# Optimization experiments

Hardware: AMD Instinct MI355X
Metric: run time of the kernel (lower is better)

Reference implementation:

```python
import jax, jax.numpy as jnp
import numpy as np

N, E, B = 50000, 800000, 128
H, L, FIN, GF = 256, 4, 8, 85
LN_EPS = 1e-5


def _ln(x, g, b):
    m = jnp.mean(x, axis=-1, keepdims=True)
    v = jnp.var(x, axis=-1, keepdims=True)
    return g * (x - m) * jax.lax.rsqrt(v + LN_EPS) + b


def setup_inputs() -> dict:
    key = jax.random.key(0)
    ks = iter(jax.random.split(key, 40))

    def nrm(shape, scale):
        return jax.random.normal(next(ks), shape, jnp.float32) * scale

    inp = {}
    inp["x"] = nrm((N, FIN), 1.0)
    inp["edge_index"] = jax.random.randint(next(ks), (2, E), 0, N, dtype=jnp.int32)
    inp["edge_weight"] = jax.random.uniform(next(ks), (E,), jnp.float32)
    inp["batch"] = jnp.sort(jax.random.randint(next(ks), (N,), 0, B, dtype=jnp.int32))
    inp["gene_feat"] = nrm((B, GF), 1.0)
    # input projection
    inp["W_in"] = nrm((FIN, H), FIN ** -0.5); inp["b_in"] = jnp.zeros((H,), jnp.float32)
    inp["ln_in_g"] = jnp.ones((H,), jnp.float32); inp["ln_in_b"] = jnp.zeros((H,), jnp.float32)
    # GIN layers (stacked over L)
    inp["eps"] = jnp.zeros((L,), jnp.float32)
    inp["W1"] = nrm((L, H, 2 * H), H ** -0.5); inp["b1"] = jnp.zeros((L, 2 * H), jnp.float32)
    inp["W2"] = nrm((L, 2 * H, H), (2 * H) ** -0.5); inp["b2"] = jnp.zeros((L, H), jnp.float32)
    inp["ln_g"] = jnp.ones((L, H), jnp.float32); inp["ln_b"] = jnp.zeros((L, H), jnp.float32)
    # gene feature projection
    inp["Wg1"] = nrm((GF, H), GF ** -0.5); inp["bg1"] = jnp.zeros((H,), jnp.float32)
    inp["lng_g"] = jnp.ones((H,), jnp.float32); inp["lng_b"] = jnp.zeros((H,), jnp.float32)
    inp["Wg2"] = nrm((H, H // 2), H ** -0.5); inp["bg2"] = jnp.zeros((H // 2,), jnp.float32)
    # classifier (embed_dim = 2H + H//2 = 640)
    ED = 2 * H + H // 2
    inp["Wc1"] = nrm((ED, H), ED ** -0.5); inp["bc1"] = jnp.zeros((H,), jnp.float32)
    inp["Wc2"] = nrm((H, H // 2), H ** -0.5); inp["bc2"] = jnp.zeros((H // 2,), jnp.float32)
    inp["Wc3"] = nrm((H // 2, 2), (H // 2) ** -0.5); inp["bc3"] = jnp.zeros((2,), jnp.float32)
    return inp


def reference(x, edge_index, edge_weight, batch, gene_feat,
              W_in, b_in, ln_in_g, ln_in_b,
              eps, W1, b1, W2, b2, ln_g, ln_b,
              Wg1, bg1, lng_g, lng_b, Wg2, bg2,
              Wc1, bc1, Wc2, bc2, Wc3, bc3):
    n = x.shape[0]
    nb = gene_feat.shape[0]
    # input projection: Linear -> LayerNorm -> ReLU  (dropout = eval mode)
    h = jax.nn.relu(_ln(x @ W_in + b_in, ln_in_g, ln_in_b))
    src, dst = edge_index[0], edge_index[1]
    for i in range(W1.shape[0]):
        res = h
        # weighted GIN aggregation; self-loops with weight 1 fold into (2+eps)*h
        msg = h[src] * edge_weight[:, None]            # [E, H]
        agg = jax.ops.segment_sum(msg, dst, num_segments=n)
        out = (2.0 + eps[i]) * h + agg
        out = jax.nn.relu(out @ W1[i] + b1[i]) @ W2[i] + b2[i]
        h = jax.nn.relu(_ln(out, ln_g[i], ln_b[i])) + res
    # dual pooling (mean + max) per graph
    counts = jax.ops.segment_sum(jnp.ones((n,), h.dtype), batch, num_segments=nb)
    gmean = jax.ops.segment_sum(h, batch, num_segments=nb) / jnp.clip(counts, 1.0)[:, None]
    gmax = jax.ops.segment_max(h, batch, num_segments=nb)
    gmax = jnp.where(jnp.isfinite(gmax), gmax, 0.0)
    # gene feature projection
    gp = jax.nn.relu(_ln(gene_feat @ Wg1 + bg1, lng_g, lng_b))
    gp = jax.nn.relu(gp @ Wg2 + bg2)
    g = jnp.concatenate([gmean, gmax, gp], axis=-1)   # [B, 640]
    # classifier
    hc = jax.nn.relu(g @ Wc1 + bc1)
    hc = jax.nn.relu(hc @ Wc2 + bc2)
    return hc @ Wc3 + bc3
```

## Files before the change

### kernel.cpp

```cpp
#include <hip/hip_runtime.h>
#include <hip/hip_bf16.h>

#define N_NODES 50000
#define MP 50048
#define N_EDGES 800000
#define N_B 128
#define H_DIM 256
#define H2_DIM 512
#define FIN_DIM 8
#define GF_DIM 85
#define LN_EPS 1e-5f
#define SCAN_NBLK 196

typedef unsigned short u16;
typedef unsigned int u32;
typedef _Float16 f16;
typedef __attribute__((ext_vector_type(8))) _Float16 f16x8;
typedef __attribute__((ext_vector_type(8))) unsigned short u16x8;
typedef __attribute__((ext_vector_type(4))) float f32x4;

__device__ inline float relu_f(float x) { return x > 0.f ? x : 0.f; }

__device__ inline float h2f(u16 b) { f16 h; __builtin_memcpy(&h, &b, 2); return (float)h; }
__device__ inline u16 f2h(float x) { f16 h = (f16)x; u16 b; __builtin_memcpy(&b, &h, 2); return b; }

#define GLOAD16(gp, lp) __builtin_amdgcn_global_load_lds( \
    (const __attribute__((address_space(1))) void*)(gp),  \
    (__attribute__((address_space(3))) void*)(lp), 16, 0, 0)

__device__ inline void ln_stats_256(float v, float* sbuf, float& mean, float& rstd) {
    float s = v, s2 = v * v;
#pragma unroll
    for (int off = 32; off > 0; off >>= 1) {
        s += __shfl_down(s, off);
        s2 += __shfl_down(s2, off);
    }
    int t = threadIdx.x;
    if ((t & 63) == 0) { sbuf[t >> 6] = s; sbuf[4 + (t >> 6)] = s2; }
    __syncthreads();
    float ts = sbuf[0] + sbuf[1] + sbuf[2] + sbuf[3];
    float ts2 = sbuf[4] + sbuf[5] + sbuf[6] + sbuf[7];
    mean = ts * (1.f / H_DIM);
    float var = ts2 * (1.f / H_DIM) - mean * mean;
    rstd = rsqrtf(var + LN_EPS);
}

__global__ void k_input_proj(const float* __restrict__ x, const float* __restrict__ Wi,
                             const float* __restrict__ bi, const float* __restrict__ g,
                             const float* __restrict__ bb,
                             u16* __restrict__ Hh, u16* __restrict__ Hl) {
    int n = blockIdx.x, t = threadIdx.x;
    __shared__ float xs[FIN_DIM];
    __shared__ float sbuf[8];
    if (t < FIN_DIM) xs[t] = x[n * FIN_DIM + t];
    __syncthreads();
    float acc = bi[t];
#pragma unroll
    for (int k = 0; k < FIN_DIM; ++k) acc = fmaf(xs[k], Wi[k * H_DIM + t], acc);
    float mean, rstd;
    ln_stats_256(acc, sbuf, mean, rstd);
    float v = relu_f(g[t] * (acc - mean) * rstd + bb[t]);
    u16 hh = f2h(v);
    size_t o = (size_t)n * H_DIM + t;
    Hh[o] = hh;
    Hl[o] = f2h(v - h2f(hh));
}

__global__ void k_hist(const int* __restrict__ ei, int* __restrict__ deg) {
    int e = blockIdx.x * 256 + threadIdx.x;
    atomicAdd(&deg[ei[N_EDGES + e]], 1);
}

__global__ void k_scan1(const int* __restrict__ deg, int* __restrict__ row_start,
                        int* __restrict__ bsum) {
    __shared__ int s[256];
    int t = threadIdx.x, i = blockIdx.x * 256 + t;
    int v = (i < N_NODES) ? deg[i] : 0;
    s[t] = v;
    __syncthreads();
    for (int off = 1; off < 256; off <<= 1) {
        int x = (t >= off) ? s[t - off] : 0;
        __syncthreads();
        s[t] += x;
        __syncthreads();
    }
    if (i < N_NODES) row_start[i] = s[t] - v;
    if (t == 255) bsum[blockIdx.x] = s[255];
}

__global__ void k_scan2(int* __restrict__ bsum) {
    __shared__ int s[256];
    int t = threadIdx.x;
    int v = (t < SCAN_NBLK) ? bsum[t] : 0;
    s[t] = v;
    __syncthreads();
    for (int off = 1; off < 256; off <<= 1) {
        int x = (t >= off) ? s[t - off] : 0;
        __syncthreads();
        s[t] += x;
        __syncthreads();
    }
    if (t < SCAN_NBLK) bsum[t] = s[t] - v;
}

__global__ void k_scan3(int* __restrict__ row_start, const int* __restrict__ bsum) {
    int t = threadIdx.x, i = blockIdx.x * 256 + t;
    if (i < N_NODES) row_start[i] += bsum[blockIdx.x];
    if (i == 0) row_start[N_NODES] = N_EDGES;
}

__global__ void k_scatter(const int* __restrict__ ei, const float* __restrict__ ew,
                          const int* __restrict__ row_start, int* __restrict__ cursor,
                          int* __restrict__ csr_src, float* __restrict__ csr_w) {
    int e = blockIdx.x * 256 + threadIdx.x;
    int d = ei[N_EDGES + e];
    int p = atomicAdd(&cursor[d], 1);
    int i = row_start[d] + p;
    csr_src[i] = ei[e];
    csr_w[i] = ew[e];
}

__global__ void k_gbounds(const int* __restrict__ batch, int* __restrict__ gstart,
                          int* __restrict__ gcnt) {
    __shared__ int s[N_B + 1];
    int b = threadIdx.x;
    int lo = 0, hi = N_NODES;
    while (lo < hi) {
        int mid = (lo + hi) >> 1;
        if (batch[mid] < b) lo = mid + 1; else hi = mid;
    }
    s[b] = lo;
    if (b == 0) s[N_B] = N_NODES;
    __syncthreads();
    gstart[b] = s[b];
    gcnt[b] = s[b + 1] - s[b];
}

__global__ void k_agg(const u16* __restrict__ Hh, const u16* __restrict__ Hl,
                      const int* __restrict__ row_start,
                      const int* __restrict__ csr_src, const float* __restrict__ csr_w,
                      const float* __restrict__ eps, int layer,
                      u16* __restrict__ Ah) {
    const int n = blockIdx.x, t = threadIdx.x, wv = t >> 6, lane = t & 63;
    const int half = lane >> 5, sl = lane & 31;
    __shared__ int s_src[256];
    __shared__ float s_w[256];
    __shared__ float part[4][256];
    int start = row_start[n], end = row_start[n + 1];
    float a[8];
#pragma unroll
    for (int q = 0; q < 8; ++q) a[q] = 0.f;
    for (int e0 = start; e0 < end; e0 += 256) {
        int ne = end - e0; if (ne > 256) ne = 256;
        if (t < ne) { s_src[t] = csr_src[e0 + t]; s_w[t] = csr_w[e0 + t]; }
        __syncthreads();
        for (int j = wv * 2 + half; j < ne; j += 8) {
            int src = s_src[j];
            float w = s_w[j];
            u16x8 v = *reinterpret_cast<const u16x8*>(&Hh[(size_t)src * H_DIM + sl * 8]);
#pragma unroll
            for (int q = 0; q < 8; ++q) a[q] = fmaf(w, h2f(v[q]), a[q]);
        }
        __syncthreads();
    }
#pragma unroll
    for (int q = 0; q < 8; ++q) a[q] += __shfl_xor(a[q], 32);
    if (half == 0) {
        *reinterpret_cast<float4*>(&part[wv][sl * 8]) = (float4){a[0], a[1], a[2], a[3]};
        *reinterpret_cast<float4*>(&part[wv][sl * 8 + 4]) = (float4){a[4], a[5], a[6], a[7]};
    }
    __syncthreads();
    float sum = part[0][t] + part[1][t] + part[2][t] + part[3][t];
    size_t so = (size_t)n * H_DIM + t;
    float e2 = 2.0f + eps[layer];
    float hs = h2f(Hh[so]) + h2f(Hl[so]);
    Ah[so] = f2h(e2 * hs + sum);
}

__global__ void k_wprep(const float* __restrict__ W, u16* __restrict__ T, int R, int C) {
    __shared__ float tile[64][65];
    int c0 = blockIdx.x * 64, r0 = blockIdx.y * 64;
    const float* Wl = W + (size_t)blockIdx.z * R * C;
    u16* Tl_ = T + (size_t)blockIdx.z * R * C;
    int t = threadIdx.x;
    int col = t & 63, qr = t >> 6;
#pragma unroll
    for (int i = 0; i < 16; ++i) {
        int row = i * 4 + qr;
        tile[row][col] = Wl[(size_t)(r0 + row) * C + c0 + col];
    }
    __syncthreads();
#pragma unroll
    for (int i = 0; i < 16; ++i) {
        int crow = i * 4 + qr;
        Tl_[(size_t)(c0 + crow) * R + r0 + col] = f2h(tile[col][crow]);
    }
}

#define C1LD 520
__global__ __launch_bounds__(512, 2) void k_mlp(
    const u16* __restrict__ Ah, const u16* __restrict__ W1t, const u16* __restrict__ W2t,
    const float* __restrict__ b1v, const float* __restrict__ b2v,
    const float* __restrict__ lg, const float* __restrict__ lbv,
    const u16* __restrict__ Rh, const u16* __restrict__ Rl,
    u16* __restrict__ Oh, u16* __restrict__ Ol) {
    __shared__ __align__(16) u16 sA[64 * 32];
    __shared__ __align__(16) u16 sB[512 * 32];
    __shared__ __align__(16) u16 sC1[64 * C1LD];
    __shared__ float lnS[64][4], lnS2[64][4];
    __shared__ float lnm[64], lnr[64];
    const int t = threadIdx.x;
    const int wv = t >> 6, lane = t & 63;
    const int fr = lane & 15, kg = lane >> 4;
    const int cg = wv & 3, rg = wv >> 2;
    const int m0 = blockIdx.x * 64;

    f32x4 acc1[2][8];
#pragma unroll
    for (int i = 0; i < 2; ++i)
#pragma unroll
        for (int j = 0; j < 8; ++j) acc1[i][j] = (f32x4){0.f, 0.f, 0.f, 0.f};

    for (int k0 = 0; k0 < H_DIM; k0 += 32) {
        if (wv < 4) {
            int r = t >> 2, p = t & 3;
            GLOAD16(Ah + (size_t)(m0 + r) * H_DIM + k0 + p * 8, &sA[(wv * 64) * 8]);
        }
#pragma unroll
        for (int is = 0; is < 4; ++is) {
            int chunk = is * 512 + t;
            int r = chunk >> 2, p = chunk & 3;
            GLOAD16(W1t + (size_t)r * H_DIM + k0 + p * 8, &sB[(is * 512 + wv * 64) * 8]);
        }
        __syncthreads();
        f16x8 fa[2], fb[8];
#pragma unroll
        for (int mf = 0; mf < 2; ++mf)
            fa[mf] = *(const f16x8*)&sA[(rg * 32 + mf * 16 + fr) * 32 + kg * 8];
#pragma unroll
        for (int nf = 0; nf < 8; ++nf)
            fb[nf] = *(const f16x8*)&sB[(cg * 128 + nf * 16 + fr) * 32 + kg * 8];
#pragma unroll
        for (int mf = 0; mf < 2; ++mf)
#pragma unroll
            for (int nf = 0; nf < 8; ++nf)
                acc1[mf][nf] = __builtin_amdgcn_mfma_f32_16x16x32_f16(fa[mf], fb[nf], acc1[mf][nf], 0, 0, 0);
        __syncthreads();
    }
#pragma unroll
    for (int nf = 0; nf < 8; ++nf) {
        int col = cg * 128 + nf * 16 + fr;
        float bi = b1v[col];
#pragma unroll
        for (int mf = 0; mf < 2; ++mf)
#pragma unroll
            for (int j = 0; j < 4; ++j) {
                int row = rg * 32 + mf * 16 + kg * 4 + j;
                sC1[row * C1LD + col] = f2h(relu_f(acc1[mf][nf][j] + bi));
            }
    }
    __syncthreads();

    f32x4 acc2[2][4];
#pragma unroll
    for (int i = 0; i < 2; ++i)
#pragma unroll
        for (int j = 0; j < 4; ++j) acc2[i][j] = (f32x4){0.f, 0.f, 0.f, 0.f};

    for (int k0 = 0; k0 < H2_DIM; k0 += 32) {
#pragma unroll
        for (int is = 0; is < 2; ++is) {
            int chunk = is * 512 + t;
            int r = chunk >> 2, p = chunk & 3;
            GLOAD16(W2t + (size_t)r * H2_DIM + k0 + p * 8, &sB[(is * 512 + wv * 64) * 8]);
        }
        __syncthreads();
        f16x8 fa[2], fb[4];
#pragma unroll
        for (int mf = 0; mf < 2; ++mf)
            fa[mf] = *(const f16x8*)&sC1[(rg * 32 + mf * 16 + fr) * C1LD + k0 + kg * 8];
#pragma unroll
        for (int nf = 0; nf < 4; ++nf)
            fb[nf] = *(const f16x8*)&sB[(cg * 64 + nf * 16 + fr) * 32 + kg * 8];
#pragma unroll
        for (int mf = 0; mf < 2; ++mf)
#pragma unroll
            for (int nf = 0; nf < 4; ++nf)
                acc2[mf][nf] = __builtin_amdgcn_mfma_f32_16x16x32_f16(fa[mf], fb[nf], acc2[mf][nf], 0, 0, 0);
        __syncthreads();
    }
    float bcol[4];
#pragma unroll
    for (int nf = 0; nf < 4; ++nf) bcol[nf] = b2v[cg * 64 + nf * 16 + fr];
#pragma unroll
    for (int mf = 0; mf < 2; ++mf)
#pragma unroll
        for (int nf = 0; nf < 4; ++nf)
#pragma unroll
            for (int j = 0; j < 4; ++j) acc2[mf][nf][j] += bcol[nf];
#pragma unroll
    for (int mf = 0; mf < 2; ++mf)
#pragma unroll
        for (int j = 0; j < 4; ++j) {
            float s = acc2[mf][0][j] + acc2[mf][1][j] + acc2[mf][2][j] + acc2[mf][3][j];
            float s2 = acc2[mf][0][j] * acc2[mf][0][j] + acc2[mf][1][j] * acc2[mf][1][j] +
                       acc2[mf][2][j] * acc2[mf][2][j] + acc2[mf][3][j] * acc2[mf][3][j];
#pragma unroll
            for (int off = 1; off < 16; off <<= 1) {
                s += __shfl_xor(s, off);
                s2 += __shfl_xor(s2, off);
            }
            if (fr == 0) {
                int row = rg * 32 + mf * 16 + kg * 4 + j;
                lnS[row][cg] = s;
                lnS2[row][cg] = s2;
            }
        }
    __syncthreads();
    if (t < 64) {
        float s = lnS[t][0] + lnS[t][1] + lnS[t][2] + lnS[t][3];
        float s2 = lnS2[t][0] + lnS2[t][1] + lnS2[t][2] + lnS2[t][3];
        float m = s * (1.f / 256.f);
        float var = s2 * (1.f / 256.f) - m * m;
        lnm[t] = m;
        lnr[t] = rsqrtf(var + LN_EPS);
    }
    __syncthreads();
    float gg[4], bb[4];
#pragma unroll
    for (int nf = 0; nf < 4; ++nf) {
        int col = cg * 64 + nf * 16 + fr;
        gg[nf] = lg[col];
        bb[nf] = lbv[col];
    }
#pragma unroll
    for (int mf = 0; mf < 2; ++mf)
#pragma unroll
        for (int j = 0; j < 4; ++j) {
            int row = rg * 32 + mf * 16 + kg * 4 + j;
            int grow = m0 + row;
            float m = lnm[row], rs = lnr[row];
#pragma unroll
            for (int nf = 0; nf < 4; ++nf) {
                int col = cg * 64 + nf * 16 + fr;
                size_t o = (size_t)grow * H_DIM + col;
                float res = h2f(Rh[o]) + h2f(Rl[o]);
                float v = relu_f(gg[nf] * (acc2[mf][nf][j] - m) * rs + bb[nf]) + res;
                u16 hh = f2h(v);
                Oh[o] = hh;
                Ol[o] = f2h(v - h2f(hh));
            }
        }
}

__global__ void k_pool(const u16* __restrict__ Hh, const u16* __restrict__ Hl,
                       const int* __restrict__ gstart,
                       const int* __restrict__ gcnt, float* __restrict__ g) {
    int b = blockIdx.x;
    int col = blockIdx.y * 64 + (threadIdx.x & 63);
    int r = threadIdx.x >> 6;
    int st = gstart[b], cnt = gcnt[b];
    float s = 0.f, mx = -3.4e38f;
    for (int i = r; i < cnt; i += 4) {
        size_t o = (size_t)(st + i) * H_DIM + col;
        float v = h2f(Hh[o]) + h2f(Hl[o]);
        s += v;
        mx = fmaxf(mx, v);
    }
    __shared__ float ss[256], sm[256];
    ss[threadIdx.x] = s;
    sm[threadIdx.x] = mx;
    __syncthreads();
    if (r == 0) {
#pragma unroll
        for (int k = 1; k < 4; ++k) {
            s += ss[threadIdx.x + 64 * k];
            mx = fmaxf(mx, sm[threadIdx.x + 64 * k]);
        }
        float mean = cnt > 0 ? s / (float)cnt : 0.f;
        if (cnt == 0) mx = 0.f;
        g[b * 640 + col] = mean;
        g[b * 640 + 256 + col] = mx;
    }
}

__global__ void k_gene(const float* __restrict__ gf, const float* __restrict__ Wg1,
                       const float* __restrict__ bg1, const float* __restrict__ lg,
                       const float* __restrict__ lb, const float* __restrict__ Wg2,
                       const float* __restrict__ bg2, float* __restrict__ g) {
    int b = blockIdx.x, t = threadIdx.x;
    __shared__ float xs[GF_DIM];
    __shared__ float sbuf[8];
    __shared__ float s1[H_DIM];
    if (t < GF_DIM) xs[t] = gf[b * GF_DIM + t];
    __syncthreads();
    float acc = bg1[t];
    for (int k = 0; k < GF_DIM; ++k) acc = fmaf(xs[k], Wg1[k * H_DIM + t], acc);
    float mean, rstd;
    ln_stats_256(acc, sbuf, mean, rstd);
    s1[t] = relu_f(lg[t] * (acc - mean) * rstd + lb[t]);
    __syncthreads();
    if (t < 128) {
        float a2 = bg2[t];
        for (int k = 0; k < H_DIM; ++k) a2 = fmaf(s1[k], Wg2[k * 128 + t], a2);
        g[b * 640 + 512 + t] = relu_f(a2);
    }
}

__global__ void k_cls(const float* __restrict__ g, const float* __restrict__ Wc1,
                      const float* __restrict__ bc1, const float* __restrict__ Wc2,
                      const float* __restrict__ bc2, const float* __restrict__ Wc3,
                      const float* __restrict__ bc3, float* __restrict__ out) {
    int b = blockIdx.x, t = threadIdx.x;
    __shared__ float gg[640];
    __shared__ float s1[256];
    __shared__ float s2[128];
    gg[t] = g[b * 640 + t];
    gg[t + 256] = g[b * 640 + 256 + t];
    if (t < 128) gg[t + 512] = g[b * 640 + 512 + t];
    __syncthreads();
    float a = bc1[t];
    for (int k = 0; k < 640; ++k) a = fmaf(gg[k], Wc1[k * 256 + t], a);
    s1[t] = relu_f(a);
    __syncthreads();
    if (t < 128) {
        float a2 = bc2[t];
        for (int k = 0; k < 256; ++k) a2 = fmaf(s1[k], Wc2[k * 128 + t], a2);
        s2[t] = relu_f(a2);
    }
    __syncthreads();
    if (t < 2) {
        float a3 = bc3[t];
        for (int k = 0; k < 128; ++k) a3 = fmaf(s2[k], Wc3[k * 2 + t], a3);
        out[b * 2 + t] = a3;
    }
}

extern "C" void kernel_launch(void* const* d_in, const int* in_sizes, int n_in,
                              void* d_out, int out_size, void* d_ws, size_t ws_size,
                              hipStream_t stream) {
    const float* x = (const float*)d_in[0];
    const int* ei = (const int*)d_in[1];
    const float* ew = (const float*)d_in[2];
    const int* batch = (const int*)d_in[3];
    const float* gf = (const float*)d_in[4];
    const float* W_in = (const float*)d_in[5];
    const float* b_in = (const float*)d_in[6];
    const float* ln_in_g = (const float*)d_in[7];
    const float* ln_in_b = (const float*)d_in[8];
    const float* eps = (const float*)d_in[9];
    const float* W1 = (const float*)d_in[10];
    const float* b1 = (const float*)d_in[11];
    const float* W2 = (const float*)d_in[12];
    const float* b2 = (const float*)d_in[13];
    const float* ln_g = (const float*)d_in[14];
    const float* ln_b = (const float*)d_in[15];
    const float* Wg1 = (const float*)d_in[16];
    const float* bg1 = (const float*)d_in[17];
    const float* lng_g = (const float*)d_in[18];
    const float* lng_b = (const float*)d_in[19];
    const float* Wg2 = (const float*)d_in[20];
    const float* bg2 = (const float*)d_in[21];
    const float* Wc1 = (const float*)d_in[22];
    const float* bc1 = (const float*)d_in[23];
    const float* Wc2 = (const float*)d_in[24];
    const float* bc2 = (const float*)d_in[25];
    const float* Wc3 = (const float*)d_in[26];
    const float* bc3 = (const float*)d_in[27];
    float* out = (float*)d_out;

    char* ws = (char*)d_ws;
    size_t off = 0;
    auto alloc = [&](size_t bytes) -> char* {
        char* p = ws + off;
        off += (bytes + 255) & ~(size_t)255;
        return p;
    };
    u16* Hh0 = (u16*)alloc((size_t)MP * H_DIM * 2);
    u16* Hl0 = (u16*)alloc((size_t)MP * H_DIM * 2);
    u16* Hh1 = (u16*)alloc((size_t)MP * H_DIM * 2);
    u16* Hl1 = (u16*)alloc((size_t)MP * H_DIM * 2);
    u16* Ah = (u16*)alloc((size_t)MP * H_DIM * 2);
    u16* W1T = (u16*)alloc((size_t)4 * H2_DIM * H_DIM * 2);
    u16* W2T = (u16*)alloc((size_t)4 * H_DIM * H2_DIM * 2);
    int* deg = (int*)alloc(N_NODES * 4);
    int* cursor = (int*)alloc(N_NODES * 4);
    int* row_start = (int*)alloc((N_NODES + 1) * 4);
    int* bsum = (int*)alloc(256 * 4);
    int* gcnt = (int*)alloc(N_B * 4);
    int* gstart = (int*)alloc(N_B * 4);
    int* csr_src = (int*)alloc(N_EDGES * 4);
    float* csr_w = (float*)alloc(N_EDGES * 4);
    float* gbuf = (float*)alloc(N_B * 640 * 4);
    (void)ws_size; (void)in_sizes; (void)n_in; (void)out_size;

    hipMemsetAsync(deg, 0, (size_t)((char*)row_start - (char*)deg), stream);

    k_wprep<<<dim3(H2_DIM / 64, H_DIM / 64, 4), 256, 0, stream>>>(W1, W1T, H_DIM, H2_DIM);
    k_wprep<<<dim3(H_DIM / 64, H2_DIM / 64, 4), 256, 0, stream>>>(W2, W2T, H2_DIM, H_DIM);

    k_input_proj<<<N_NODES, 256, 0, stream>>>(x, W_in, b_in, ln_in_g, ln_in_b, Hh0, Hl0);
    k_hist<<<N_EDGES / 256, 256, 0, stream>>>(ei, deg);
    k_scan1<<<SCAN_NBLK, 256, 0, stream>>>(deg, row_start, bsum);
    k_scan2<<<1, 256, 0, stream>>>(bsum);
    k_scan3<<<SCAN_NBLK, 256, 0, stream>>>(row_start, bsum);
    k_scatter<<<N_EDGES / 256, 256, 0, stream>>>(ei, ew, row_start, cursor, csr_src, csr_w);
    k_gbounds<<<1, N_B, 0, stream>>>(batch, gstart, gcnt);

    u16* hch = Hh0; u16* hcl = Hl0;
    u16* hnh = Hh1; u16* hnl = Hl1;
    for (int l = 0; l < 4; ++l) {
        k_agg<<<N_NODES, 256, 0, stream>>>(hch, hcl, row_start, csr_src, csr_w, eps, l, Ah);
        k_mlp<<<MP / 64, 512, 0, stream>>>(
            Ah, W1T + (size_t)l * H2_DIM * H_DIM, W2T + (size_t)l * H_DIM * H2_DIM,
            b1 + (size_t)l * H2_DIM, b2 + (size_t)l * H_DIM,
            ln_g + (size_t)l * H_DIM, ln_b + (size_t)l * H_DIM,
            hch, hcl, hnh, hnl);
        u16* th = hch; hch = hnh; hnh = th;
        u16* tl = hcl; hcl = hnl; hnl = tl;
    }

    k_pool<<<dim3(N_B, 4), 256, 0, stream>>>(hch, hcl, gstart, gcnt, gbuf);
    k_gene<<<N_B, 256, 0, stream>>>(gf, Wg1, bg1, lng_g, lng_b, Wg2, bg2, gbuf);
    k_cls<<<N_B, 256, 0, stream>>>(gbuf, Wc1, bc1, Wc2, bc2, Wc3, bc3, out);
}
```

Measured before the change: 910.9 us.

## Halve MLP row tile to 32 and XOR-swizzle the intermediate LDS buffer

```diff
diff --git a/kernel.cpp b/kernel.cpp
--- a/kernel.cpp
+++ b/kernel.cpp
@@ -197,34 +197,32 @@
     }
 }
 
-#define C1LD 520
+#define C1IDX(row, k) (((row) * 512 + (k)) ^ (((row) & 7) << 3))
 __global__ __launch_bounds__(512, 2) void k_mlp(
     const u16* __restrict__ Ah, const u16* __restrict__ W1t, const u16* __restrict__ W2t,
     const float* __restrict__ b1v, const float* __restrict__ b2v,
     const float* __restrict__ lg, const float* __restrict__ lbv,
     const u16* __restrict__ Rh, const u16* __restrict__ Rl,
     u16* __restrict__ Oh, u16* __restrict__ Ol) {
-    __shared__ __align__(16) u16 sA[64 * 32];
+    __shared__ __align__(16) u16 sA[32 * 32];
     __shared__ __align__(16) u16 sB[512 * 32];
-    __shared__ __align__(16) u16 sC1[64 * C1LD];
-    __shared__ float lnS[64][4], lnS2[64][4];
-    __shared__ float lnm[64], lnr[64];
+    __shared__ __align__(16) u16 sC1[32 * 512];
+    __shared__ float lnS[32][4], lnS2[32][4];
+    __shared__ float lnm[32], lnr[32];
     const int t = threadIdx.x;
     const int wv = t >> 6, lane = t & 63;
     const int fr = lane & 15, kg = lane >> 4;
     const int cg = wv & 3, rg = wv >> 2;
-    const int m0 = blockIdx.x * 64;
-
-    f32x4 acc1[2][8];
-#pragma unroll
-    for (int i = 0; i < 2; ++i)
-#pragma unroll
-        for (int j = 0; j < 8; ++j) acc1[i][j] = (f32x4){0.f, 0.f, 0.f, 0.f};
+    const int m0 = blockIdx.x * 32;
+
+    f32x4 acc1[8];
+#pragma unroll
+    for (int j = 0; j < 8; ++j) acc1[j] = (f32x4){0.f, 0.f, 0.f, 0.f};
 
     for (int k0 = 0; k0 < H_DIM; k0 += 32) {
-        if (wv < 4) {
+        if (t < 128) {
             int r = t >> 2, p = t & 3;
-            GLOAD16(Ah + (size_t)(m0 + r) * H_DIM + k0 + p * 8, &sA[(wv * 64) * 8]);
+            GLOAD16(Ah + (size_t)(m0 + r) * H_DIM + k0 + p * 8, &sA[wv * 512]);
         }
 #pragma unroll
         for (int is = 0; is < 4; ++is) {
@@ -233,18 +231,14 @@
             GLOAD16(W1t + (size_t)r * H_DIM + k0 + p * 8, &sB[(is * 512 + wv * 64) * 8]);
         }
         __syncthreads();
-        f16x8 fa[2], fb[8];
-#pragma unroll
-        for (int mf = 0; mf < 2; ++mf)
-            fa[mf] = *(const f16x8*)&sA[(rg * 32 + mf * 16 + fr) * 32 + kg * 8];
+        f16x8 fa, fb[8];
+        fa = *(const f16x8*)&sA[(rg * 16 + fr) * 32 + kg * 8];
 #pragma unroll
         for (int nf = 0; nf < 8; ++nf)
             fb[nf] = *(const f16x8*)&sB[(cg * 128 + nf * 16 + fr) * 32 + kg * 8];
 #pragma unroll
-        for (int mf = 0; mf < 2; ++mf)
-#pragma unroll
-            for (int nf = 0; nf < 8; ++nf)
-                acc1[mf][nf] = __builtin_amdgcn_mfma_f32_16x16x32_f16(fa[mf], fb[nf], acc1[mf][nf], 0, 0, 0);
+        for (int nf = 0; nf < 8; ++nf)
+            acc1[nf] = __builtin_amdgcn_mfma_f32_16x16x32_f16(fa, fb[nf], acc1[nf], 0, 0, 0);
         __syncthreads();
     }
 #pragma unroll
@@ -252,20 +246,16 @@
         int col = cg * 128 + nf * 16 + fr;
         float bi = b1v[col];
 #pragma unroll
-        for (int mf = 0; mf < 2; ++mf)
-#pragma unroll
-            for (int j = 0; j < 4; ++j) {
-                int row = rg * 32 + mf * 16 + kg * 4 + j;
-                sC1[row * C1LD + col] = f2h(relu_f(acc1[mf][nf][j] + bi));
-            }
-    }
-    __syncthreads();
-
-    f32x4 acc2[2][4];
-#pragma unroll
-    for (int i = 0; i < 2; ++i)
-#pragma unroll
-        for (int j = 0; j < 4; ++j) acc2[i][j] = (f32x4){0.f, 0.f, 0.f, 0.f};
+        for (int j = 0; j < 4; ++j) {
+            int row = rg * 16 + kg * 4 + j;
+            sC1[C1IDX(row, col)] = f2h(relu_f(acc1[nf][j] + bi));
+        }
+    }
+    __syncthreads();
+
+    f32x4 acc2[4];
+#pragma unroll
+    for (int j = 0; j < 4; ++j) acc2[j] = (f32x4){0.f, 0.f, 0.f, 0.f};
 
     for (int k0 = 0; k0 < H2_DIM; k0 += 32) {
 #pragma unroll
@@ -275,49 +265,44 @@
             GLOAD16(W2t + (size_t)r * H2_DIM + k0 + p * 8, &sB[(is * 512 + wv * 64) * 8]);
         }
         __syncthreads();
-        f16x8 fa[2], fb[4];
-#pragma unroll
-        for (int mf = 0; mf < 2; ++mf)
-            fa[mf] = *(const f16x8*)&sC1[(rg * 32 + mf * 16 + fr) * C1LD + k0 + kg * 8];
+        f16x8 fa, fb[4];
+        {
+            int row = rg * 16 + fr;
+            fa = *(const f16x8*)&sC1[C1IDX(row, k0 + kg * 8)];
+        }
 #pragma unroll
         for (int nf = 0; nf < 4; ++nf)
             fb[nf] = *(const f16x8*)&sB[(cg * 64 + nf * 16 + fr) * 32 + kg * 8];
 #pragma unroll
-        for (int mf = 0; mf < 2; ++mf)
-#pragma unroll
-            for (int nf = 0; nf < 4; ++nf)
-                acc2[mf][nf] = __builtin_amdgcn_mfma_f32_16x16x32_f16(fa[mf], fb[nf], acc2[mf][nf], 0, 0, 0);
+        for (int nf = 0; nf < 4; ++nf)
+            acc2[nf] = __builtin_amdgcn_mfma_f32_16x16x32_f16(fa, fb[nf], acc2[nf], 0, 0, 0);
         __syncthreads();
     }
     float bcol[4];
 #pragma unroll
     for (int nf = 0; nf < 4; ++nf) bcol[nf] = b2v[cg * 64 + nf * 16 + fr];
 #pragma unroll
-    for (int mf = 0; mf < 2; ++mf)
-#pragma unroll
-        for (int nf = 0; nf < 4; ++nf)
-#pragma unroll
-            for (int j = 0; j < 4; ++j) acc2[mf][nf][j] += bcol[nf];
-#pragma unroll
-    for (int mf = 0; mf < 2; ++mf)
-#pragma unroll
-        for (int j = 0; j < 4; ++j) {
-            float s = acc2[mf][0][j] + acc2[mf][1][j] + acc2[mf][2][j] + acc2[mf][3][j];
-            float s2 = acc2[mf][0][j] * acc2[mf][0][j] + acc2[mf][1][j] * acc2[mf][1][j] +
-                       acc2[mf][2][j] * acc2[mf][2][j] + acc2[mf][3][j] * acc2[mf][3][j];
-#pragma unroll
-            for (int off = 1; off < 16; off <<= 1) {
-                s += __shfl_xor(s, off);
-                s2 += __shfl_xor(s2, off);
-            }
-            if (fr == 0) {
-                int row = rg * 32 + mf * 16 + kg * 4 + j;
-                lnS[row][cg] = s;
-                lnS2[row][cg] = s2;
-            }
-        }
-    __syncthreads();
-    if (t < 64) {
+    for (int nf = 0; nf < 4; ++nf)
+#pragma unroll
+        for (int j = 0; j < 4; ++j) acc2[nf][j] += bcol[nf];
+#pragma unroll
+    for (int j = 0; j < 4; ++j) {
+        float s = acc2[0][j] + acc2[1][j] + acc2[2][j] + acc2[3][j];
+        float s2 = acc2[0][j] * acc2[0][j] + acc2[1][j] * acc2[1][j] +
+                   acc2[2][j] * acc2[2][j] + acc2[3][j] * acc2[3][j];
+#pragma unroll
+        for (int off = 1; off < 16; off <<= 1) {
+            s += __shfl_xor(s, off);
+            s2 += __shfl_xor(s2, off);
+        }
+        if (fr == 0) {
+            int row = rg * 16 + kg * 4 + j;
+            lnS[row][cg] = s;
+            lnS2[row][cg] = s2;
+        }
+    }
+    __syncthreads();
+    if (t < 32) {
         float s = lnS[t][0] + lnS[t][1] + lnS[t][2] + lnS[t][3];
         float s2 = lnS2[t][0] + lnS2[t][1] + lnS2[t][2] + lnS2[t][3];
         float m = s * (1.f / 256.f);
@@ -334,23 +319,21 @@
         bb[nf] = lbv[col];
     }
 #pragma unroll
-    for (int mf = 0; mf < 2; ++mf)
-#pragma unroll
-        for (int j = 0; j < 4; ++j) {
-            int row = rg * 32 + mf * 16 + kg * 4 + j;
-            int grow = m0 + row;
-            float m = lnm[row], rs = lnr[row];
-#pragma unroll
-            for (int nf = 0; nf < 4; ++nf) {
-                int col = cg * 64 + nf * 16 + fr;
-                size_t o = (size_t)grow * H_DIM + col;
-                float res = h2f(Rh[o]) + h2f(Rl[o]);
-                float v = relu_f(gg[nf] * (acc2[mf][nf][j] - m) * rs + bb[nf]) + res;
-                u16 hh = f2h(v);
-                Oh[o] = hh;
-                Ol[o] = f2h(v - h2f(hh));
-            }
-        }
+    for (int j = 0; j < 4; ++j) {
+        int row = rg * 16 + kg * 4 + j;
+        int grow = m0 + row;
+        float m = lnm[row], rs = lnr[row];
+#pragma unroll
+        for (int nf = 0; nf < 4; ++nf) {
+            int col = cg * 64 + nf * 16 + fr;
+            size_t o = (size_t)grow * H_DIM + col;
+            float res = h2f(Rh[o]) + h2f(Rl[o]);
+            float v = relu_f(gg[nf] * (acc2[nf][j] - m) * rs + bb[nf]) + res;
+            u16 hh = f2h(v);
+            Oh[o] = hh;
+            Ol[o] = f2h(v - h2f(hh));
+        }
+    }
 }
 
 __global__ void k_pool(const u16* __restrict__ Hh, const u16* __restrict__ Hl,
@@ -511,7 +494,7 @@
     u16* hnh = Hh1; u16* hnl = Hl1;
     for (int l = 0; l < 4; ++l) {
         k_agg<<<N_NODES, 256, 0, stream>>>(hch, hcl, row_start, csr_src, csr_w, eps, l, Ah);
-        k_mlp<<<MP / 64, 512, 0, stream>>>(
+        k_mlp<<<MP / 32, 512, 0, stream>>>(
             Ah, W1T + (size_t)l * H2_DIM * H_DIM, W2T + (size_t)l * H_DIM * H2_DIM,
             b1 + (size_t)l * H2_DIM, b2 + (size_t)l * H_DIM,
             ln_g + (size_t)l * H_DIM, ln_b + (size_t)l * H_DIM,
```

Result: faster. 872.7 us (-4.2%).

## Restructure fused MLP: 32-row tiles, weights straight from global, swizzled LDS

Applied to the files above, without the earlier changes.

```diff
diff --git a/kernel.cpp b/kernel.cpp
--- a/kernel.cpp
+++ b/kernel.cpp
@@ -197,139 +197,139 @@
     }
 }
 
-#define C1LD 520
+#define C1IDX(row, k) (((row) * 512 + (k)) ^ (((row) & 7) << 3))
 __global__ __launch_bounds__(512, 2) void k_mlp(
     const u16* __restrict__ Ah, const u16* __restrict__ W1t, const u16* __restrict__ W2t,
     const float* __restrict__ b1v, const float* __restrict__ b2v,
     const float* __restrict__ lg, const float* __restrict__ lbv,
     const u16* __restrict__ Rh, const u16* __restrict__ Rl,
     u16* __restrict__ Oh, u16* __restrict__ Ol) {
-    __shared__ __align__(16) u16 sA[64 * 32];
-    __shared__ __align__(16) u16 sB[512 * 32];
-    __shared__ __align__(16) u16 sC1[64 * C1LD];
-    __shared__ float lnS[64][4], lnS2[64][4];
-    __shared__ float lnm[64], lnr[64];
+    __shared__ __align__(16) u16 sA[32 * 256];
+    __shared__ __align__(16) u16 sC1[32 * 512];
+    __shared__ float lnS[32][8], lnS2[32][8];
+    __shared__ float lnm[32], lnr[32];
     const int t = threadIdx.x;
     const int wv = t >> 6, lane = t & 63;
     const int fr = lane & 15, kg = lane >> 4;
-    const int cg = wv & 3, rg = wv >> 2;
-    const int m0 = blockIdx.x * 64;
-
-    f32x4 acc1[2][8];
+    const int m0 = blockIdx.x * 32;
+
+#pragma unroll
+    for (int i = 0; i < 2; ++i) {
+        int chunk = i * 512 + t;
+        int r = chunk >> 5, c = chunk & 31;
+        GLOAD16(Ah + (size_t)(m0 + r) * H_DIM + ((c ^ (r & 7)) << 3),
+                &sA[(i * 512 + wv * 64) * 8]);
+    }
+    __syncthreads();
+
+    f32x4 acc1[2][4];
 #pragma unroll
     for (int i = 0; i < 2; ++i)
 #pragma unroll
-        for (int j = 0; j < 8; ++j) acc1[i][j] = (f32x4){0.f, 0.f, 0.f, 0.f};
-
-    for (int k0 = 0; k0 < H_DIM; k0 += 32) {
-        if (wv < 4) {
-            int r = t >> 2, p = t & 3;
-            GLOAD16(Ah + (size_t)(m0 + r) * H_DIM + k0 + p * 8, &sA[(wv * 64) * 8]);
-        }
-#pragma unroll
-        for (int is = 0; is < 4; ++is) {
-            int chunk = is * 512 + t;
-            int r = chunk >> 2, p = chunk & 3;
-            GLOAD16(W1t + (size_t)r * H_DIM + k0 + p * 8, &sB[(is * 512 + wv * 64) * 8]);
-        }
-        __syncthreads();
-        f16x8 fa[2], fb[8];
+        for (int j = 0; j < 4; ++j) acc1[i][j] = (f32x4){0.f, 0.f, 0.f, 0.f};
+
+#pragma unroll 2
+    for (int step = 0; step < 8; ++step) {
+        int k0 = step * 32;
+        f16x8 fa[2], fb[4];
+#pragma unroll
+        for (int mf = 0; mf < 2; ++mf) {
+            int row = mf * 16 + fr;
+            int cc = (step * 4 + kg) ^ (row & 7);
+            fa[mf] = *(const f16x8*)&sA[row * 256 + cc * 8];
+        }
+#pragma unroll
+        for (int nf = 0; nf < 4; ++nf) {
+            int col = wv * 64 + nf * 16 + fr;
+            fb[nf] = *(const f16x8*)&W1t[(size_t)col * H_DIM + k0 + kg * 8];
+        }
 #pragma unroll
         for (int mf = 0; mf < 2; ++mf)
-            fa[mf] = *(const f16x8*)&sA[(rg * 32 + mf * 16 + fr) * 32 + kg * 8];
-#pragma unroll
-        for (int nf = 0; nf < 8; ++nf)
-            fb[nf] = *(const f16x8*)&sB[(cg * 128 + nf * 16 + fr) * 32 + kg * 8];
+#pragma unroll
+            for (int nf = 0; nf < 4; ++nf)
+                acc1[mf][nf] = __builtin_amdgcn_mfma_f32_16x16x32_f16(fa[mf], fb[nf], acc1[mf][nf], 0, 0, 0);
+    }
+#pragma unroll
+    for (int nf = 0; nf < 4; ++nf) {
+        int col = wv * 64 + nf * 16 + fr;
+        float bi = b1v[col];
 #pragma unroll
         for (int mf = 0; mf < 2; ++mf)
 #pragma unroll
-            for (int nf = 0; nf < 8; ++nf)
-                acc1[mf][nf] = __builtin_amdgcn_mfma_f32_16x16x32_f16(fa[mf], fb[nf], acc1[mf][nf], 0, 0, 0);
-        __syncthreads();
-    }
-#pragma unroll
-    for (int nf = 0; nf < 8; ++nf) {
-        int col = cg * 128 + nf * 16 + fr;
-        float bi = b1v[col];
+            for (int j = 0; j < 4; ++j) {
+                int row = mf * 16 + kg * 4 + j;
+                sC1[C1IDX(row, col)] = f2h(relu_f(acc1[mf][nf][j] + bi));
+            }
+    }
+    __syncthreads();
+
+    f32x4 acc2[2][2];
+#pragma unroll
+    for (int i = 0; i < 2; ++i)
+#pragma unroll
+        for (int j = 0; j < 2; ++j) acc2[i][j] = (f32x4){0.f, 0.f, 0.f, 0.f};
+
+#pragma unroll 2
+    for (int step = 0; step < 16; ++step) {
+        int k0 = step * 32;
+        f16x8 fa[2], fb[2];
+#pragma unroll
+        for (int mf = 0; mf < 2; ++mf) {
+            int row = mf * 16 + fr;
+            fa[mf] = *(const f16x8*)&sC1[C1IDX(row, k0 + kg * 8)];
+        }
+#pragma unroll
+        for (int nf = 0; nf < 2; ++nf) {
+            int col = wv * 32 + nf * 16 + fr;
+            fb[nf] = *(const f16x8*)&W2t[(size_t)col * H2_DIM + k0 + kg * 8];
+        }
 #pragma unroll
         for (int mf = 0; mf < 2; ++mf)
 #pragma unroll
-            for (int j = 0; j < 4; ++j) {
-                int row = rg * 32 + mf * 16 + kg * 4 + j;
-                sC1[row * C1LD + col] = f2h(relu_f(acc1[mf][nf][j] + bi));
-            }
-    }
-    __syncthreads();
-
-    f32x4 acc2[2][4];
-#pragma unroll
-    for (int i = 0; i < 2; ++i)
-#pragma unroll
-        for (int j = 0; j < 4; ++j) acc2[i][j] = (f32x4){0.f, 0.f, 0.f, 0.f};
-
-    for (int k0 = 0; k0 < H2_DIM; k0 += 32) {
-#pragma unroll
-        for (int is = 0; is < 2; ++is) {
-            int chunk = is * 512 + t;
-            int r = chunk >> 2, p = chunk & 3;
-            GLOAD16(W2t + (size_t)r * H2_DIM + k0 + p * 8, &sB[(is * 512 + wv * 64) * 8]);
-        }
-        __syncthreads();
-        f16x8 fa[2], fb[4];
-#pragma unroll
-        for (int mf = 0; mf < 2; ++mf)
-            fa[mf] = *(const f16x8*)&sC1[(rg * 32 + mf * 16 + fr) * C1LD + k0 + kg * 8];
-#pragma unroll
-        for (int nf = 0; nf < 4; ++nf)
-            fb[nf] = *(const f16x8*)&sB[(cg * 64 + nf * 16 + fr) * 32 + kg * 8];
-#pragma unroll
-        for (int mf = 0; mf < 2; ++mf)
-#pragma unroll
-            for (int nf = 0; nf < 4; ++nf)
+            for (int nf = 0; nf < 2; ++nf)
                 acc2[mf][nf] = __builtin_amdgcn_mfma_f32_16x16x32_f16(fa[mf], fb[nf], acc2[mf][nf], 0, 0, 0);
-        __syncthreads();
-    }
-    float bcol[4];
-#pragma unroll
-    for (int nf = 0; nf < 4; ++nf) bcol[nf] = b2v[cg * 64 + nf * 16 + fr];
+    }
+    float bcol[2];
+#pragma unroll
+    for (int nf = 0; nf < 2; ++nf) bcol[nf] = b2v[wv * 32 + nf * 16 + fr];
 #pragma unroll
     for (int mf = 0; mf < 2; ++mf)
 #pragma unroll
-        for (int nf = 0; nf < 4; ++nf)
+        for (int nf = 0; nf < 2; ++nf)
 #pragma unroll
             for (int j = 0; j < 4; ++j) acc2[mf][nf][j] += bcol[nf];
 #pragma unroll
     for (int mf = 0; mf < 2; ++mf)
 #pragma unroll
         for (int j = 0; j < 4; ++j) {
-            float s = acc2[mf][0][j] + acc2[mf][1][j] + acc2[mf][2][j] + acc2[mf][3][j];
-            float s2 = acc2[mf][0][j] * acc2[mf][0][j] + acc2[mf][1][j] * acc2[mf][1][j] +
-                       acc2[mf][2][j] * acc2[mf][2][j] + acc2[mf][3][j] * acc2[mf][3][j];
+            float s = acc2[mf][0][j] + acc2[mf][1][j];
+            float s2 = acc2[mf][0][j] * acc2[mf][0][j] + acc2[mf][1][j] * acc2[mf][1][j];
 #pragma unroll
             for (int off = 1; off < 16; off <<= 1) {
                 s += __shfl_xor(s, off);
                 s2 += __shfl_xor(s2, off);
             }
             if (fr == 0) {
-                int row = rg * 32 + mf * 16 + kg * 4 + j;
-                lnS[row][cg] = s;
-                lnS2[row][cg] = s2;
+                int row = mf * 16 + kg * 4 + j;
+                lnS[row][wv] = s;
+                lnS2[row][wv] = s2;
             }
         }
     __syncthreads();
-    if (t < 64) {
-        float s = lnS[t][0] + lnS[t][1] + lnS[t][2] + lnS[t][3];
-        float s2 = lnS2[t][0] + lnS2[t][1] + lnS2[t][2] + lnS2[t][3];
+    if (t < 32) {
+        float s = 0.f, s2 = 0.f;
+#pragma unroll
+        for (int w = 0; w < 8; ++w) { s += lnS[t][w]; s2 += lnS2[t][w]; }
         float m = s * (1.f / 256.f);
         float var = s2 * (1.f / 256.f) - m * m;
         lnm[t] = m;
         lnr[t] = rsqrtf(var + LN_EPS);
     }
     __syncthreads();
-    float gg[4], bb[4];
-#pragma unroll
-    for (int nf = 0; nf < 4; ++nf) {
-        int col = cg * 64 + nf * 16 + fr;
+    float gg[2], bb[2];
+#pragma unroll
+    for (int nf = 0; nf < 2; ++nf) {
+        int col = wv * 32 + nf * 16 + fr;
         gg[nf] = lg[col];
         bb[nf] = lbv[col];
     }
@@ -337,12 +337,12 @@
     for (int mf = 0; mf < 2; ++mf)
 #pragma unroll
         for (int j = 0; j < 4; ++j) {
-            int row = rg * 32 + mf * 16 + kg * 4 + j;
+            int row = mf * 16 + kg * 4 + j;
             int grow = m0 + row;
             float m = lnm[row], rs = lnr[row];
 #pragma unroll
-            for (int nf = 0; nf < 4; ++nf) {
-                int col = cg * 64 + nf * 16 + fr;
+            for (int nf = 0; nf < 2; ++nf) {
+                int col = wv * 32 + nf * 16 + fr;
                 size_t o = (size_t)grow * H_DIM + col;
                 float res = h2f(Rh[o]) + h2f(Rl[o]);
                 float v = relu_f(gg[nf] * (acc2[mf][nf][j] - m) * rs + bb[nf]) + res;
@@ -511,7 +511,7 @@
     u16* hnh = Hh1; u16* hnl = Hl1;
     for (int l = 0; l < 4; ++l) {
         k_agg<<<N_NODES, 256, 0, stream>>>(hch, hcl, row_start, csr_src, csr_w, eps, l, Ah);
-        k_mlp<<<MP / 64, 512, 0, stream>>>(
+        k_mlp<<<MP / 32, 512, 0, stream>>>(
             Ah, W1T + (size_t)l * H2_DIM * H_DIM, W2T + (size_t)l * H_DIM * H2_DIM,
             b1 + (size_t)l * H2_DIM, b2 + (size_t)l * H_DIM,
             ln_g + (size_t)l * H_DIM, ln_b + (size_t)l * H_DIM,
```

After: 965.4 us. 6.0% more time.
